# Kernel optimization log

Measured on AMD Instinct MI355X. Metric: run time of the kernel, lower is better.

Reference implementation:

```python
import jax, jax.numpy as jnp
import numpy as np

SOW_INIT = 1e-10  # sum_of_weights_initial_value
EPS = 1e-8       # torch.nn.CosineSimilarity default eps


def setup_inputs() -> dict:
    key = jax.random.key(0)
    k1, k2, k3 = jax.random.split(key, 3)
    input_image = jax.random.normal(k1, (1, 3, 224, 224), dtype=jnp.float32)
    masks = jax.random.uniform(k2, (1000, 224, 224), dtype=jnp.float32)
    # Linear encoder: flattened image [3*224*224] -> feature dim 128
    W = jax.random.normal(k3, (3, 224, 224, 128), dtype=jnp.float32) * 0.01
    return {"input_image": input_image, "masks": masks, "W": W}


def reference(input_image, masks, W):
    img = input_image[0]  # [3, H, W]
    # Encoder applied to (img * mask): rep_n = sum_chw (img*mask)[c,h,w] * W[c,h,w,f]
    # Precompute A[h,w,f] = sum_c img[c,h,w] * W[c,h,w,f] so masked reps never
    # materialize the [N,3,H,W] masked-image tensor.
    A = jnp.einsum('chw,chwf->hwf', img, W)          # [H, W, F]
    rep0 = jnp.sum(A, axis=(0, 1))                   # unmasked representation [F]
    reps = jnp.einsum('nhw,hwf->nf', masks, A)       # masked representations [N, F]

    # Cosine similarity (dim=1), clamped norms as in torch
    n0 = jnp.maximum(jnp.linalg.norm(rep0), EPS)
    nr = jnp.maximum(jnp.linalg.norm(reps, axis=1), EPS)
    sims = (reps @ rep0) / (nr * n0)                 # [N]

    H, Wd = masks.shape[1], masks.shape[2]
    imp0 = jnp.zeros((H, Wd), dtype=jnp.float32)
    unc0 = jnp.zeros((H, Wd), dtype=jnp.float32)
    sow0 = jnp.full((H, Wd), SOW_INIT, dtype=jnp.float32)

    def step(carry, inp):
        imp, unc, sow = carry
        m, s = inp  # mask [H,W], similarity scalar
        sow = sow + m
        prev = imp
        imp = imp + m * (s - imp) / sow
        unc = unc + (s - imp) * (s - prev) * m
        return (imp, unc, sow), None

    (imp, unc, sow), _ = jax.lax.scan(step, (imp0, unc0, sow0), (masks, sims))
    return jnp.stack([imp, unc, sow])  # [3, H, W]
```

## Files before the change

### kernel.cpp

```cpp
#include <hip/hip_runtime.h>
#include <hip/hip_bf16.h>
#include <stdint.h>

#define HWN 50176
#define NM  1000
#define FD  128
#define NSPLIT 49
#define KSTEPS 32
#define NSCAN 20
#define NPB 50

typedef __attribute__((ext_vector_type(8))) short short8;
typedef __attribute__((ext_vector_type(4))) float f32x4;

__device__ __forceinline__ unsigned short f2bf(float x) {
    union { float f; unsigned u; } v; v.f = x;
    unsigned r = v.u + 0x7FFFu + ((v.u >> 16) & 1u);
    return (unsigned short)(r >> 16);
}

#define AS1(p) ((const __attribute__((address_space(1))) unsigned int*)(p))
#define AS3(p) ((__attribute__((address_space(3))) unsigned int*)(p))

__global__ __launch_bounds__(256) void k_encode(const float* __restrict__ img,
                                                const float* __restrict__ Wt,
                                                unsigned short* __restrict__ Bpack,
                                                float* __restrict__ rep0part)
{
    const int t = threadIdx.x;
    const int f = t & 127;
    const int kt = blockIdx.x * 2 + (t >> 7);
    const int hw0 = kt * 32;
    float vals[32];
    float rsum = 0.f;
#pragma unroll
    for (int e = 0; e < 32; ++e) {
        const int hw = hw0 + e;
        float a = img[hw] * __builtin_nontemporal_load(Wt + (size_t)hw * FD + f);
        a = fmaf(img[HWN + hw],     __builtin_nontemporal_load(Wt + (size_t)(HWN + hw) * FD + f), a);
        a = fmaf(img[2 * HWN + hw], __builtin_nontemporal_load(Wt + (size_t)(2 * HWN + hw) * FD + f), a);
        vals[e] = a;
        rsum += a;
    }
    char* tile = (char*)Bpack + (size_t)kt * 8192;
#pragma unroll
    for (int j = 0; j < 4; ++j) {
        short8 pk;
#pragma unroll
        for (int e = 0; e < 8; ++e) pk[e] = (short)f2bf(vals[j * 8 + e]);
        const int slot = (f * 4 + j) ^ ((f >> 1) & 3);
        *reinterpret_cast<short8*>(tile + (slot << 4)) = pk;
    }
    __shared__ float red[256];
    red[t] = rsum;
    __syncthreads();
    if (t < 128) rep0part[(size_t)blockIdx.x * 128 + f] = red[t] + red[t + 128];
}

__global__ __launch_bounds__(256) void k_rep0red(const float* __restrict__ rep0part,
                                                 float* __restrict__ rep0)
{
    const int f = blockIdx.x;
    float s = 0.f;
    for (int b = threadIdx.x; b < 784; b += 256) s += rep0part[(size_t)b * 128 + f];
    __shared__ float red[256];
    red[threadIdx.x] = s;
    __syncthreads();
    for (int o = 128; o > 0; o >>= 1) {
        if (threadIdx.x < o) red[threadIdx.x] += red[threadIdx.x + o];
        __syncthreads();
    }
    if (threadIdx.x == 0) rep0[f] = red[0];
}

__global__ __launch_bounds__(256, 4) void k_gemm(const float* __restrict__ masks,
                                                 const unsigned short* __restrict__ Bpack,
                                                 float* __restrict__ partial)
{
    __shared__ __align__(16) char Bs[3][8192];

    const int t = threadIdx.x;
    const int wv = t >> 6, lane = t & 63;
    const int lrow = lane & 15, kg = lane >> 4;

    const int bid = blockIdx.x;
    const int swz = (bid & 7) * 98 + (bid >> 3);
    const int split = swz >> 4, mtile = swz & 15;
    const int n0 = mtile * 64;

    int row = n0 + wv * 16 + lrow;
    if (row >= NM) row = NM - 1;
    const float* aSrc = masks + (size_t)row * HWN + split * 1024 + kg * 8;
    const char*  bSrc = (const char*)Bpack + (size_t)split * (KSTEPS * 8192) + t * 16;

    int bo[8];
#pragma unroll
    for (int ft = 0; ft < 8; ++ft) {
        const int f = ft * 16 + lrow;
        bo[ft] = ((f * 4 + kg) ^ ((f >> 1) & 3)) << 4;
    }

    f32x4 acc[8];
#pragma unroll
    for (int i = 0; i < 8; ++i) acc[i] = f32x4{0.f, 0.f, 0.f, 0.f};

    f32x4 aA0, aA1, aB0, aB1, aC0, aC1;

#define STAGE(KS, BUFOFF) do {                                                                     \
        __builtin_amdgcn_global_load_lds(AS1(bSrc + (size_t)(KS) * 8192),        AS3(&Bs[0][0] + (BUFOFF) + ((t & 255) * 16)), 16, 0, 0); \
        __builtin_amdgcn_global_load_lds(AS1(bSrc + (size_t)(KS) * 8192 + 4096), AS3(&Bs[0][0] + (BUFOFF) + 4096 + ((t & 255) * 16)), 16, 0, 0); \
    } while (0)

    __builtin_amdgcn_sched_barrier(0);
    STAGE(0, 0);
    aA0 = *reinterpret_cast<const f32x4*>(aSrc);
    aA1 = *reinterpret_cast<const f32x4*>(aSrc + 4);
    __builtin_amdgcn_sched_barrier(0);
    STAGE(1, 8192);
    aB0 = *reinterpret_cast<const f32x4*>(aSrc + 32);
    aB1 = *reinterpret_cast<const f32x4*>(aSrc + 36);
    __builtin_amdgcn_sched_barrier(0);

    int boff_c = 0;
    for (int ks = 0; ks < KSTEPS; ++ks) {
        const int boff_s = (boff_c + 16384 >= 24576) ? (boff_c + 16384 - 24576) : (boff_c + 16384);
        if (ks + 2 < KSTEPS) {
            __builtin_amdgcn_sched_barrier(0);
            STAGE(ks + 2, boff_s);
            aC0 = *reinterpret_cast<const f32x4*>(aSrc + (ks + 2) * 32);
            aC1 = *reinterpret_cast<const f32x4*>(aSrc + (ks + 2) * 32 + 4);
            __builtin_amdgcn_sched_barrier(0);
            asm volatile("s_waitcnt vmcnt(8)" ::: "memory");
        } else if (ks == KSTEPS - 2) {
            asm volatile("s_waitcnt vmcnt(4)" ::: "memory");
        } else {
            asm volatile("s_waitcnt vmcnt(0)" ::: "memory");
        }
        __builtin_amdgcn_s_barrier();
        __builtin_amdgcn_sched_barrier(0);

        const char* B = &Bs[0][0] + boff_c;
        short8 bfv[8];
#pragma unroll
        for (int ft = 0; ft < 8; ++ft)
            bfv[ft] = *reinterpret_cast<const short8*>(B + bo[ft]);

        union { short8 s; __hip_bfloat162 h[4]; } apk;
        apk.h[0] = __float22bfloat162_rn(float2{aA0[0], aA0[1]});
        apk.h[1] = __float22bfloat162_rn(float2{aA0[2], aA0[3]});
        apk.h[2] = __float22bfloat162_rn(float2{aA1[0], aA1[1]});
        apk.h[3] = __float22bfloat162_rn(float2{aA1[2], aA1[3]});

        asm volatile("s_waitcnt lgkmcnt(0)" ::: "memory");
        __builtin_amdgcn_sched_barrier(0);
        __builtin_amdgcn_s_setprio(1);
#pragma unroll
        for (int ft = 0; ft < 8; ++ft)
            acc[ft] = __builtin_amdgcn_mfma_f32_16x16x32_bf16(apk.s, bfv[ft], acc[ft], 0, 0, 0);
        __builtin_amdgcn_s_setprio(0);
        __builtin_amdgcn_sched_barrier(0);
        if (ks + 1 < KSTEPS) {
            __builtin_amdgcn_s_barrier();
            __builtin_amdgcn_sched_barrier(0);
        }
        aA0 = aB0; aA1 = aB1; aB0 = aC0; aB1 = aC1;
        boff_c = (boff_c + 8192 >= 24576) ? 0 : (boff_c + 8192);
    }
#undef STAGE

    const int crow = n0 + wv * 16 + (kg << 2);
    float* pb = partial + ((size_t)split * 1024 + crow) * FD + lrow;
#pragma unroll
    for (int ft = 0; ft < 8; ++ft)
#pragma unroll
        for (int rr = 0; rr < 4; ++rr)
            __builtin_nontemporal_store(acc[ft][rr], pb + (size_t)rr * FD + ft * 16);
}

__global__ __launch_bounds__(128) void k_sims(const float* __restrict__ partial,
                                              const float* __restrict__ rep0,
                                              float* __restrict__ sims)
{
    const int n = blockIdx.x;
    const int f = threadIdx.x;
    float rsum = 0.f;
    for (int s = 0; s < NSPLIT; ++s)
        rsum += __builtin_nontemporal_load(partial + ((size_t)s * 1024 + n) * FD + f);
    const float r0 = rep0[f];
    __shared__ float red0[128], red1[128], red2[128];
    red0[f] = rsum * r0;
    red1[f] = rsum * rsum;
    red2[f] = r0 * r0;
    __syncthreads();
    for (int o = 64; o > 0; o >>= 1) {
        if (f < o) {
            red0[f] += red0[f + o];
            red1[f] += red1[f + o];
            red2[f] += red2[f + o];
        }
        __syncthreads();
    }
    if (f == 0) {
        const float nr = fmaxf(sqrtf(red1[0]), 1e-8f);
        const float nz = fmaxf(sqrtf(red2[0]), 1e-8f);
        sims[n] = red0[0] / (nr * nz);
    }
}

__global__ __launch_bounds__(256) void k_colsums(const float* __restrict__ masks,
                                                 const float* __restrict__ sims,
                                                 float* __restrict__ Spart)
{
    __shared__ float s1v[NPB], s2v[NPB];
    const int t = threadIdx.x;
    const int split = blockIdx.y;
    if (t < NPB) {
        const float s = sims[split * NPB + t];
        s1v[t] = s;
        s2v[t] = s * s;
    }
    __syncthreads();
    const int pix = (blockIdx.x * 256 + t) * 4;
    const float* mp = masks + (size_t)split * NPB * HWN + pix;
    f32x4 s0 = {0.f,0.f,0.f,0.f}, s1 = s0, s2 = s0;
#pragma unroll 5
    for (int i = 0; i < NPB; ++i) {
        const f32x4 m = *reinterpret_cast<const f32x4*>(mp + (size_t)i * HWN);
        const float a = s1v[i], b = s2v[i];
        s0 += m;
#pragma unroll
        for (int e = 0; e < 4; ++e) {
            s1[e] = fmaf(m[e], a, s1[e]);
            s2[e] = fmaf(m[e], b, s2[e]);
        }
    }
    float* sp = Spart + (size_t)split * 3 * HWN + pix;
    __builtin_nontemporal_store(s0, reinterpret_cast<f32x4*>(sp));
    __builtin_nontemporal_store(s1, reinterpret_cast<f32x4*>(sp + HWN));
    __builtin_nontemporal_store(s2, reinterpret_cast<f32x4*>(sp + 2 * HWN));
}

__global__ __launch_bounds__(256) void k_final(const float* __restrict__ Spart,
                                               float* __restrict__ out)
{
    const int pix = (blockIdx.x * 256 + threadIdx.x) * 4;
    f32x4 s0 = {0.f,0.f,0.f,0.f}, s1 = s0, s2 = s0;
#pragma unroll 4
    for (int sp = 0; sp < NSCAN; ++sp) {
        const float* p = Spart + (size_t)sp * 3 * HWN + pix;
        s0 += __builtin_nontemporal_load(reinterpret_cast<const f32x4*>(p));
        s1 += __builtin_nontemporal_load(reinterpret_cast<const f32x4*>(p + HWN));
        s2 += __builtin_nontemporal_load(reinterpret_cast<const f32x4*>(p + 2 * HWN));
    }
    f32x4 imp, unc, sow;
#pragma unroll
    for (int e = 0; e < 4; ++e) {
        sow[e] = 1e-10f + s0[e];
        imp[e] = s1[e] / sow[e];
        unc[e] = fmaf(-imp[e], s1[e], s2[e]);
    }
    *reinterpret_cast<f32x4*>(out + pix) = imp;
    *reinterpret_cast<f32x4*>(out + HWN + pix) = unc;
    *reinterpret_cast<f32x4*>(out + 2 * HWN + pix) = sow;
}

extern "C" void kernel_launch(void* const* d_in, const int* in_sizes, int n_in,
                              void* d_out, int out_size, void* d_ws, size_t ws_size,
                              hipStream_t stream) {
    const float* img   = (const float*)d_in[0];
    const float* masks = (const float*)d_in[1];
    const float* Wt    = (const float*)d_in[2];
    float* out = (float*)d_out;

    char* ws = (char*)d_ws;
    unsigned short* Bpack = (unsigned short*)ws;
    float* partial  = (float*)(ws + 12845056);
    float* rep0part = partial;
    float* rep0     = (float*)(ws + 38535168);
    float* sims     = (float*)(ws + 38535680);
    float* Spart    = (float*)ws;

    hipLaunchKernelGGL(k_encode,  dim3(784), dim3(256), 0, stream, img, Wt, Bpack, rep0part);
    hipLaunchKernelGGL(k_rep0red, dim3(128), dim3(256), 0, stream, rep0part, rep0);
    hipLaunchKernelGGL(k_gemm,    dim3(784), dim3(256), 0, stream, masks, Bpack, partial);
    hipLaunchKernelGGL(k_sims,    dim3(NM), dim3(128), 0, stream, partial, rep0, sims);
    hipLaunchKernelGGL(k_colsums, dim3(49, NSCAN), dim3(256), 0, stream, masks, sims, Spart);
    hipLaunchKernelGGL(k_final,   dim3(49), dim3(256), 0, stream, Spart, out);
}
```

Baseline: 123.2 us.

## Split mask GEMM into single-wave blocks with barrier-free double buffering

Replaces the 4-wave, 64-row GEMM block with a one-wave block that handles 16 mask rows. Each wave now loads the full bf16 B tile into its own double-buffered LDS and sync is done only with vmcnt waits, with no s_barrier. The grid grows to 3087 blocks, with an XCD-aware swizzle over split and row-group. This removes inter-wave barrier stalls and raises the number of independent blocks. The cost is that each B tile is now re-read from L2 four times as often, because waves no longer share it.

```diff
diff --git a/kernel.cpp b/kernel.cpp
--- a/kernel.cpp
+++ b/kernel.cpp
@@ -7,6 +7,7 @@
 #define FD  128
 #define NSPLIT 49
 #define KSTEPS 32
+#define NRG 63
 #define NSCAN 20
 #define NPB 50
 
@@ -73,25 +74,25 @@
     if (threadIdx.x == 0) rep0[f] = red[0];
 }
 
-__global__ __launch_bounds__(256, 4) void k_gemm(const float* __restrict__ masks,
-                                                 const unsigned short* __restrict__ Bpack,
-                                                 float* __restrict__ partial)
-{
-    __shared__ __align__(16) char Bs[3][8192];
-
-    const int t = threadIdx.x;
-    const int wv = t >> 6, lane = t & 63;
+__global__ __launch_bounds__(64, 2) void k_gemm(const float* __restrict__ masks,
+                                                const unsigned short* __restrict__ Bpack,
+                                                float* __restrict__ partial)
+{
+    __shared__ __align__(16) char Blds[2][8192];
+
+    const int lane = threadIdx.x & 63;
     const int lrow = lane & 15, kg = lane >> 4;
 
     const int bid = blockIdx.x;
-    const int swz = (bid & 7) * 98 + (bid >> 3);
-    const int split = swz >> 4, mtile = swz & 15;
-    const int n0 = mtile * 64;
-
-    int row = n0 + wv * 16 + lrow;
+    const int xcd = bid & 7, idx = bid >> 3;
+    const int swz = (xcd < 7 ? xcd * 386 : 2702) + idx;
+    const int split = swz / NRG, rg = swz - split * NRG;
+    const int n0 = rg * 16;
+
+    int row = n0 + lrow;
     if (row >= NM) row = NM - 1;
     const float* aSrc = masks + (size_t)row * HWN + split * 1024 + kg * 8;
-    const char*  bSrc = (const char*)Bpack + (size_t)split * (KSTEPS * 8192) + t * 16;
+    const char*  bSrc = (const char*)Bpack + (size_t)split * (KSTEPS * 8192) + lane * 16;
 
     int bo[8];
 #pragma unroll
@@ -104,71 +105,56 @@
 #pragma unroll
     for (int i = 0; i < 8; ++i) acc[i] = f32x4{0.f, 0.f, 0.f, 0.f};
 
-    f32x4 aA0, aA1, aB0, aB1, aC0, aC1;
-
-#define STAGE(KS, BUFOFF) do {                                                                     \
-        __builtin_amdgcn_global_load_lds(AS1(bSrc + (size_t)(KS) * 8192),        AS3(&Bs[0][0] + (BUFOFF) + ((t & 255) * 16)), 16, 0, 0); \
-        __builtin_amdgcn_global_load_lds(AS1(bSrc + (size_t)(KS) * 8192 + 4096), AS3(&Bs[0][0] + (BUFOFF) + 4096 + ((t & 255) * 16)), 16, 0, 0); \
+    f32x4 aE0, aE1, aO0, aO1;
+
+#define STAGE(KS, P, AR0, AR1) do {                                                        \
+        const char* bs_ = bSrc + (size_t)(KS) * 8192;                                      \
+        _Pragma("unroll")                                                                  \
+        for (int j = 0; j < 8; ++j)                                                        \
+            __builtin_amdgcn_global_load_lds(AS1(bs_ + j * 1024),                          \
+                AS3(&Blds[P][0] + j * 1024 + lane * 16), 16, 0, 0);                        \
+        AR0 = *reinterpret_cast<const f32x4*>(aSrc + (KS) * 32);                           \
+        AR1 = *reinterpret_cast<const f32x4*>(aSrc + (KS) * 32 + 4);                       \
     } while (0)
 
-    __builtin_amdgcn_sched_barrier(0);
-    STAGE(0, 0);
-    aA0 = *reinterpret_cast<const f32x4*>(aSrc);
-    aA1 = *reinterpret_cast<const f32x4*>(aSrc + 4);
-    __builtin_amdgcn_sched_barrier(0);
-    STAGE(1, 8192);
-    aB0 = *reinterpret_cast<const f32x4*>(aSrc + 32);
-    aB1 = *reinterpret_cast<const f32x4*>(aSrc + 36);
-    __builtin_amdgcn_sched_barrier(0);
-
-    int boff_c = 0;
-    for (int ks = 0; ks < KSTEPS; ++ks) {
-        const int boff_s = (boff_c + 16384 >= 24576) ? (boff_c + 16384 - 24576) : (boff_c + 16384);
+#define COMPUTE(P, A0, A1) do {                                                            \
+        short8 bfv[8];                                                                     \
+        _Pragma("unroll")                                                                  \
+        for (int ft = 0; ft < 8; ++ft)                                                     \
+            bfv[ft] = *reinterpret_cast<const short8*>(&Blds[P][0] + bo[ft]);              \
+        union { short8 s; __hip_bfloat162 h[4]; } apk;                                     \
+        apk.h[0] = __float22bfloat162_rn(float2{A0[0], A0[1]});                            \
+        apk.h[1] = __float22bfloat162_rn(float2{A0[2], A0[3]});                            \
+        apk.h[2] = __float22bfloat162_rn(float2{A1[0], A1[1]});                            \
+        apk.h[3] = __float22bfloat162_rn(float2{A1[2], A1[3]});                            \
+        __builtin_amdgcn_s_setprio(1);                                                     \
+        _Pragma("unroll")                                                                  \
+        for (int ft = 0; ft < 8; ++ft)                                                     \
+            acc[ft] = __builtin_amdgcn_mfma_f32_16x16x32_bf16(apk.s, bfv[ft], acc[ft], 0, 0, 0); \
+        __builtin_amdgcn_s_setprio(0);                                                     \
+    } while (0)
+
+    STAGE(0, 0, aE0, aE1);
+#pragma unroll 1
+    for (int ks2 = 0; ks2 < KSTEPS / 2; ++ks2) {
+        const int ks = 2 * ks2;
+        STAGE(ks + 1, 1, aO0, aO1);
+        asm volatile("s_waitcnt vmcnt(10)" ::: "memory");
+        __builtin_amdgcn_sched_barrier(0);
+        COMPUTE(0, aE0, aE1);
         if (ks + 2 < KSTEPS) {
-            __builtin_amdgcn_sched_barrier(0);
-            STAGE(ks + 2, boff_s);
-            aC0 = *reinterpret_cast<const f32x4*>(aSrc + (ks + 2) * 32);
-            aC1 = *reinterpret_cast<const f32x4*>(aSrc + (ks + 2) * 32 + 4);
-            __builtin_amdgcn_sched_barrier(0);
-            asm volatile("s_waitcnt vmcnt(8)" ::: "memory");
-        } else if (ks == KSTEPS - 2) {
-            asm volatile("s_waitcnt vmcnt(4)" ::: "memory");
+            STAGE(ks + 2, 0, aE0, aE1);
+            asm volatile("s_waitcnt vmcnt(10)" ::: "memory");
         } else {
             asm volatile("s_waitcnt vmcnt(0)" ::: "memory");
         }
-        __builtin_amdgcn_s_barrier();
         __builtin_amdgcn_sched_barrier(0);
-
-        const char* B = &Bs[0][0] + boff_c;
-        short8 bfv[8];
-#pragma unroll
-        for (int ft = 0; ft < 8; ++ft)
-            bfv[ft] = *reinterpret_cast<const short8*>(B + bo[ft]);
-
-        union { short8 s; __hip_bfloat162 h[4]; } apk;
-        apk.h[0] = __float22bfloat162_rn(float2{aA0[0], aA0[1]});
-        apk.h[1] = __float22bfloat162_rn(float2{aA0[2], aA0[3]});
-        apk.h[2] = __float22bfloat162_rn(float2{aA1[0], aA1[1]});
-        apk.h[3] = __float22bfloat162_rn(float2{aA1[2], aA1[3]});
-
-        asm volatile("s_waitcnt lgkmcnt(0)" ::: "memory");
-        __builtin_amdgcn_sched_barrier(0);
-        __builtin_amdgcn_s_setprio(1);
-#pragma unroll
-        for (int ft = 0; ft < 8; ++ft)
-            acc[ft] = __builtin_amdgcn_mfma_f32_16x16x32_bf16(apk.s, bfv[ft], acc[ft], 0, 0, 0);
-        __builtin_amdgcn_s_setprio(0);
-        __builtin_amdgcn_sched_barrier(0);
-        if (ks + 1 < KSTEPS) {
-            __builtin_amdgcn_s_barrier();
-            __builtin_amdgcn_sched_barrier(0);
-        }
-        aA0 = aB0; aA1 = aB1; aB0 = aC0; aB1 = aC1;
-        boff_c = (boff_c + 8192 >= 24576) ? 0 : (boff_c + 8192);
+        COMPUTE(1, aO0, aO1);
     }
 #undef STAGE
-
-    const int crow = n0 + wv * 16 + (kg << 2);
+#undef COMPUTE
+
+    const int crow = n0 + (kg << 2);
     float* pb = partial + ((size_t)split * 1024 + crow) * FD + lrow;
 #pragma unroll
     for (int ft = 0; ft < 8; ++ft)
@@ -282,7 +268,7 @@
 
     hipLaunchKernelGGL(k_encode,  dim3(784), dim3(256), 0, stream, img, Wt, Bpack, rep0part);
     hipLaunchKernelGGL(k_rep0red, dim3(128), dim3(256), 0, stream, rep0part, rep0);
-    hipLaunchKernelGGL(k_gemm,    dim3(784), dim3(256), 0, stream, masks, Bpack, partial);
+    hipLaunchKernelGGL(k_gemm,    dim3(3087), dim3(64), 0, stream, masks, Bpack, partial);
     hipLaunchKernelGGL(k_sims,    dim3(NM), dim3(128), 0, stream, partial, rep0, sims);
     hipLaunchKernelGGL(k_colsums, dim3(49, NSCAN), dim3(256), 0, stream, masks, sims, Spart);
     hipLaunchKernelGGL(k_final,   dim3(49), dim3(256), 0, stream, Spart, out);
```

Result: slower. 134.3 us (+9.0%).
